# Kernel optimization log

Measured on AMD Instinct MI355X. Metric: run time of the kernel, lower is better.

Reference implementation:

```python
import jax, jax.numpy as jnp
import numpy as np

N_FACTORS = (50, 50, 50)   # vocab factorization, prod = 125000
EMB_STD = (0.5 / 512) ** (1.0 / 3.0)   # per-core std so full embedding std ~= 0.5/embedding_dim
CTX_STD = (1e-6) ** (1.0 / 3.0)


def _tt_gather(core1, core2, core3, idx):
    """idx: flat int array (N,). Cores: (n_k, r_in, m_k, r_out). Returns (N, m1*m2*m3)."""
    n1, n2, n3 = N_FACTORS
    i3 = idx % n3
    i2 = (idx // n3) % n2
    i1 = idx // (n2 * n3)
    N = idx.shape[0]
    g1 = core1[i1][:, 0]                  # (N, m1, r1)  (leading rank is 1)
    g2 = core2[i2]                        # (N, r1, m2, r2)
    res = jnp.einsum('bmr,brns->bmns', g1, g2).reshape(N, -1, g2.shape[-1])  # (N, m1*m2, r2)
    g3 = core3[i3]                        # (N, r2, m3, 1)
    res = jnp.einsum('bmr,brns->bmns', res, g3).reshape(N, -1)               # (N, m1*m2*m3)
    return res


def setup_inputs() -> dict:
    key = jax.random.key(0)
    ks = jax.random.split(key, 8)
    vocab = 125000
    word_indices = jax.random.randint(ks[0], (8192, 1), 0, vocab, dtype=jnp.int64 if jax.config.jax_enable_x64 else jnp.int32)
    context_indices = jax.random.randint(ks[1], (8192, 10), 0, vocab, dtype=jnp.int64 if jax.config.jax_enable_x64 else jnp.int32)
    w_core1 = jax.random.normal(ks[2], (50, 1, 8, 32), dtype=jnp.float32) * EMB_STD
    w_core2 = jax.random.normal(ks[3], (50, 32, 8, 32), dtype=jnp.float32) * EMB_STD
    w_core3 = jax.random.normal(ks[4], (50, 32, 8, 1), dtype=jnp.float32) * EMB_STD
    c_core1 = jax.random.normal(ks[5], (50, 1, 8, 32), dtype=jnp.float32) * CTX_STD
    c_core2 = jax.random.normal(ks[6], (50, 32, 8, 32), dtype=jnp.float32) * CTX_STD
    c_core3 = jax.random.normal(ks[7], (50, 32, 8, 1), dtype=jnp.float32) * CTX_STD
    return {
        'word_indices': word_indices,
        'context_indices': context_indices,
        'w_core1': w_core1, 'w_core2': w_core2, 'w_core3': w_core3,
        'c_core1': c_core1, 'c_core2': c_core2, 'c_core3': c_core3,
    }


def reference(word_indices, context_indices, w_core1, w_core2, w_core3, c_core1, c_core2, c_core3):
    # w = self.w_emb.forward(word_indices)[:, 0, :]
    w = _tt_gather(w_core1, w_core2, w_core3, word_indices[:, 0])          # (B, 512)
    # context_indices is 2-D: flatten, lookup, reshape back
    bs, num = context_indices.shape
    c = _tt_gather(c_core1, c_core2, c_core3, context_indices.reshape(-1)) # (B*num, 512)
    c = c.reshape(bs, num, -1)
    return (w, c)
```

## Files before the change

### kernel.cpp

```cpp
#include <hip/hip_runtime.h>


#define NFAC 50
#define TPAIR 2048
#define NPAIRS 2500
#define NKEYS 5000
#define MAXC 192
#define NWORD 8192
#define NCTX  81920
#define NLOOK (NWORD + NCTX)
#define NBB   ((NLOOK + 255) / 256)
#define NE2   409600

typedef short short8 __attribute__((ext_vector_type(8)));
typedef float f32x4v __attribute__((ext_vector_type(4)));
typedef unsigned short us4 __attribute__((ext_vector_type(4)));

__device__ __forceinline__ unsigned short f2bf(float f) {
    unsigned u = __builtin_bit_cast(unsigned, f);
    u += 0x7FFFu + ((u >> 16) & 1u);
    return (unsigned short)(u >> 16);
}

__device__ __forceinline__ int pair_of(int idx) {
    const int i3 = idx % NFAC;
    const int i2 = (idx / NFAC) % NFAC;
    return i2 * NFAC + i3;
}


__global__ __launch_bounds__(256) void tt_bucket(
    const int* __restrict__ widx, const int* __restrict__ cidx,
    const float* __restrict__ w1, const float* __restrict__ c1,
    const float* __restrict__ w2, const float* __restrict__ c2,
    const float* __restrict__ w3, const float* __restrict__ c3,
    int* __restrict__ hist, unsigned* __restrict__ bucket,
    unsigned short* __restrict__ g1w, unsigned short* __restrict__ g1c,
    unsigned short* __restrict__ g2w, unsigned short* __restrict__ g2c,
    unsigned short* __restrict__ g3w, unsigned short* __restrict__ g3c)
{
    const int b = blockIdx.x;
    const int t = threadIdx.x;
    if (b < NBB) {
        const int g = b * 256 + t;
        const int idx = (g < NWORD) ? widx[g] : cidx[g - NWORD];
        const int key = (g < NWORD ? 0 : NPAIRS) + pair_of(idx);
        const int i1  = idx / (NFAC * NFAC);
        const int pos = atomicAdd(&hist[key], 1);
        if (pos < MAXC)
            bucket[(size_t)key * MAXC + pos] = (unsigned)g | ((unsigned)i1 << 17);
        return;
    }
    if (b < NBB + 800) {
        const int gid = (b - NBB) * 256 + t;
        const int e = gid * 4;
        const float* src; unsigned short* dst; int off;
        if (e < NE2) { src = w2; dst = g2w; off = e; }
        else         { src = c2; dst = g2c; off = e - NE2; }
        const float4 v = *reinterpret_cast<const float4*>(src + off);
        us4 o; o[0] = f2bf(v.x); o[1] = f2bf(v.y); o[2] = f2bf(v.z); o[3] = f2bf(v.w);
        *reinterpret_cast<us4*>(dst + off) = o;
        return;
    }
    if (b < NBB + 900) {
        const int g = (b - NBB - 800) * 256 + t;
        if (g < 12800) g1w[g] = f2bf(w1[g]);
        else           g1c[g - 12800] = f2bf(c1[g - 12800]);
        return;
    }
    {
        const int g = (b - NBB - 900) * 256 + t;
        const int tab = g / 25600;
        const int rem = g - tab * 25600;
        const int i3 = rem >> 9, le = rem & 511;
        const int l = le >> 3, j = le & 7;
        const int col = l & 15, k = 8 * (l >> 4) + j;
        const float* src = tab ? c3 : w3;
        unsigned short* dst = tab ? g3c : g3w;
        dst[i3 * 512 + le] = (col < 8) ? f2bf(src[i3 * 256 + k * 8 + col]) : 0;
    }
}


__global__ __launch_bounds__(256, 8) void tt_group_fused(
    const unsigned* __restrict__ bucket, const int* __restrict__ hist,
    const unsigned short* __restrict__ g1w, const unsigned short* __restrict__ g1c,
    const unsigned short* __restrict__ g2w, const unsigned short* __restrict__ g2c,
    const unsigned short* __restrict__ g3w, const unsigned short* __restrict__ g3c,
    float* __restrict__ out)
{
    const int B = blockIdx.x;
    const int swz = (B & 7) * (NKEYS / 8) + (B >> 3);
    const int key = (swz & 1) ? ((swz >> 1) + NPAIRS) : (swz >> 1);

    int count = hist[key];
    if (count == 0) return;
    if (count > MAXC) count = MAXC;

    const bool isCtx = key >= NPAIRS;
    const int pair = isCtx ? key - NPAIRS : key;
    const unsigned short* g1t = isCtx ? g1c : g1w;
    const unsigned short* g2t = isCtx ? g2c : g2w;
    const unsigned short* g3t = isCtx ? g3c : g3w;
    const unsigned* kb = bucket + (size_t)key * MAXC;
    const int i2 = pair / NFAC, i3 = pair % NFAC;

    __shared__ unsigned short tl[TPAIR];
    const int t = threadIdx.x;
    const int wave = t >> 6;
    const int lane = t & 63;
    const int l15 = lane & 15;
    const int kg  = lane >> 4;

    {
        const short8 bg3 = *reinterpret_cast<const short8*>(g3t + i3 * 512 + lane * 8);
        const unsigned short* g2p = g2t + i2 * 8192;
        #pragma unroll
        for (int tile = 0; tile < 4; ++tile) {
            const int rbase = wave * 64 + tile * 16;
            const short8 a = *reinterpret_cast<const short8*>(
                g2p + (rbase + l15) * 32 + kg * 8);
            const f32x4v z = {0.f, 0.f, 0.f, 0.f};
            const f32x4v d = __builtin_amdgcn_mfma_f32_16x16x32_bf16(a, bg3, z, 0, 0, 0);
            if (l15 < 8) {
                const int p = l15;
                #pragma unroll
                for (int q = 0; q < 4; ++q) {
                    const int rn = rbase + kg * 4 + q;
                    const int r = rn >> 3, n = rn & 7;
                    const int np = n * 8 + p;
                    const int flat = (np & 3) * 512 + ((r >> 3) * 16 + (np >> 2)) * 8 + (r & 7);
                    tl[flat] = f2bf(d[q]);
                }
            }
        }
    }
    __syncthreads();

    const short8 b0 = *reinterpret_cast<const short8*>(&tl[0 * 512 + lane * 8]);
    const short8 b1 = *reinterpret_cast<const short8*>(&tl[1 * 512 + lane * 8]);
    const short8 b2 = *reinterpret_cast<const short8*>(&tl[2 * 512 + lane * 8]);
    const short8 b3 = *reinterpret_cast<const short8*>(&tl[3 * 512 + lane * 8]);

    const int sel = (lane >> 3) & 1;
    const int am  = lane & 7;

    const int ntile = (count + 1) >> 1;
    for (int jt = wave; jt < ntile; jt += 4) {
        const int j0 = 2 * jt;
        const bool has2 = (j0 + 1) < count;
        const unsigned pk0 = __builtin_amdgcn_readfirstlane(kb[j0]);
        const unsigned pk1 = has2 ? __builtin_amdgcn_readfirstlane(kb[j0 + 1]) : pk0;
        const int lid0 = pk0 & 0x1FFFF, i10 = pk0 >> 17;
        const int lid1 = pk1 & 0x1FFFF, i11 = pk1 >> 17;

        const short8 a = *reinterpret_cast<const short8*>(
            g1t + (sel ? i11 : i10) * 256 + am * 32 + kg * 8);

        const f32x4v z = {0.f, 0.f, 0.f, 0.f};
        const f32x4v d0 = __builtin_amdgcn_mfma_f32_16x16x32_bf16(a, b0, z, 0, 0, 0);
        const f32x4v d1 = __builtin_amdgcn_mfma_f32_16x16x32_bf16(a, b1, z, 0, 0, 0);
        const f32x4v d2 = __builtin_amdgcn_mfma_f32_16x16x32_bf16(a, b2, z, 0, 0, 0);
        const f32x4v d3 = __builtin_amdgcn_mfma_f32_16x16x32_bf16(a, b3, z, 0, 0, 0);

        float* o0 = out + (size_t)lid0 * 512;
        float* o1 = out + (size_t)lid1 * 512;
        #pragma unroll
        for (int q = 0; q < 4; ++q) {
            const int row = kg * 4 + q;
            const int mm = row & 7;
            float* ob = (row >= 8) ? o1 : o0;
            if (row < 8 || has2) {
                f32x4v v; v[0] = d0[q]; v[1] = d1[q]; v[2] = d2[q]; v[3] = d3[q];
                __builtin_nontemporal_store(v, (f32x4v*)(ob + mm * 64 + 4 * l15));
            }
        }
    }
}


__global__ __launch_bounds__(512) void tt_fused(
    const int* __restrict__ word_idx, const int* __restrict__ ctx_idx,
    const float* __restrict__ w1, const float* __restrict__ w2, const float* __restrict__ w3,
    const float* __restrict__ c1, const float* __restrict__ c2, const float* __restrict__ c3,
    float* __restrict__ out)
{
    const int b = blockIdx.x;
    int idx; const float *k1, *k2, *k3; float* o;
    if (b < NWORD) { idx = word_idx[b]; k1 = w1; k2 = w2; k3 = w3; o = out + (size_t)b * 512; }
    else { const int c = b - NWORD; idx = ctx_idx[c]; k1 = c1; k2 = c2; k3 = c3;
           o = out + (size_t)(NWORD + c) * 512; }
    const int i3 = idx % NFAC;
    const int rem = idx / NFAC;
    const int i2 = rem % NFAC;
    const int i1 = rem / NFAC;

    __shared__ float g3s[256];
    __shared__ float g1s[256];
    __shared__ float Ts[TPAIR];
    const int t = threadIdx.x;
    if (t < 256) g3s[t] = k3[i3 * 256 + t];
    else         g1s[t - 256] = k1[i1 * 256 + (t - 256)];
    __syncthreads();

    {
        const int e0 = t * 4;
        const int r = e0 >> 6, n = (e0 >> 3) & 7, p0 = e0 & 7;
        const float* g2row = k2 + i2 * 8192 + r * 256 + n * 32;
        float acc[4] = {0.f,0.f,0.f,0.f};
        #pragma unroll
        for (int s = 0; s < 32; ++s) {
            const float v = g2row[s];
            #pragma unroll
            for (int j = 0; j < 4; ++j) acc[j] += v * g3s[s * 8 + p0 + j];
        }
        reinterpret_cast<float4*>(Ts + e0)[0] = make_float4(acc[0], acc[1], acc[2], acc[3]);
    }
    __syncthreads();

    const int m = t >> 6, np = t & 63;
    float acc = 0.f;
    #pragma unroll
    for (int r = 0; r < 32; ++r)
        acc += g1s[m * 32 + r] * Ts[r * 64 + np];
    o[m * 64 + np] = acc;
}

extern "C" void kernel_launch(void* const* d_in, const int* in_sizes, int n_in,
                              void* d_out, int out_size, void* d_ws, size_t ws_size,
                              hipStream_t stream) {
    const int*   widx = (const int*)d_in[0];
    const int*   cidx = (const int*)d_in[1];
    const float* w1   = (const float*)d_in[2];
    const float* w2   = (const float*)d_in[3];
    const float* w3   = (const float*)d_in[4];
    const float* c1   = (const float*)d_in[5];
    const float* c2   = (const float*)d_in[6];
    const float* c3   = (const float*)d_in[7];
    float* out = (float*)d_out;

    const size_t need = 896000 * 2 + NKEYS * 4 + (size_t)NKEYS * MAXC * 4;

    if (ws_size >= need) {
        unsigned short* g1wb = (unsigned short*)d_ws;
        unsigned short* g1cb = g1wb + 12800;
        unsigned short* g2wb = g1cb + 12800;
        unsigned short* g2cb = g2wb + NE2;
        unsigned short* g3wb = g2cb + NE2;
        unsigned short* g3cb = g3wb + 25600;
        int*      hist   = (int*)(g3cb + 25600);
        unsigned* bucket = (unsigned*)(hist + NKEYS);

        hipMemsetAsync(hist, 0, NKEYS * sizeof(int), stream);
        tt_bucket<<<NBB + 1100, 256, 0, stream>>>(
            widx, cidx, w1, c1, w2, c2, w3, c3,
            hist, bucket, g1wb, g1cb, g2wb, g2cb, g3wb, g3cb);
        tt_group_fused<<<NKEYS, 256, 0, stream>>>(
            bucket, hist, g1wb, g1cb, g2wb, g2cb, g3wb, g3cb, out);
    } else {
        tt_fused<<<NLOOK, 512, 0, stream>>>(widx, cidx, w1, w2, w3, c1, c2, c3, out);
    }
}
```

Measured before the change: 61.86 us.

## Fuse memset, bucketing and grouped compute into one cooperative kernel with grid syncs

```diff
diff --git a/kernel.cpp b/kernel.cpp
--- a/kernel.cpp
+++ b/kernel.cpp
@@ -1,4 +1,5 @@
 #include <hip/hip_runtime.h>
+#include <hip/hip_cooperative_groups.h>
 
 
 #define NFAC 50
@@ -11,10 +12,14 @@
 #define NLOOK (NWORD + NCTX)
 #define NBB   ((NLOOK + 255) / 256)
 #define NE2   409600
+#define NVB   (NBB + 1100)
+#define KPX   (NKEYS / 8)
 
 typedef short short8 __attribute__((ext_vector_type(8)));
 typedef float f32x4v __attribute__((ext_vector_type(4)));
 typedef unsigned short us4 __attribute__((ext_vector_type(4)));
+
+namespace cg = cooperative_groups;
 
 __device__ __forceinline__ unsigned short f2bf(float f) {
     unsigned u = __builtin_bit_cast(unsigned, f);
@@ -29,30 +34,25 @@
 }
 
 
-__global__ __launch_bounds__(256) void tt_bucket(
-    const int* __restrict__ widx, const int* __restrict__ cidx,
-    const float* __restrict__ w1, const float* __restrict__ c1,
-    const float* __restrict__ w2, const float* __restrict__ c2,
-    const float* __restrict__ w3, const float* __restrict__ c3,
-    int* __restrict__ hist, unsigned* __restrict__ bucket,
-    unsigned short* __restrict__ g1w, unsigned short* __restrict__ g1c,
-    unsigned short* __restrict__ g2w, unsigned short* __restrict__ g2c,
-    unsigned short* __restrict__ g3w, unsigned short* __restrict__ g3c)
-{
-    const int b = blockIdx.x;
-    const int t = threadIdx.x;
-    if (b < NBB) {
-        const int g = b * 256 + t;
+__device__ __forceinline__ void do_p1(int vb, int t,
+    const int* widx, const int* cidx,
+    const float* w1, const float* c1, const float* w2, const float* c2,
+    const float* w3, const float* c3,
+    int* hist, unsigned* bucket,
+    unsigned short* g1w, unsigned short* g1c,
+    unsigned short* g2w, unsigned short* g2c,
+    unsigned short* g3w, unsigned short* g3c)
+{
+    if (vb < NBB) {
+        const int g = vb * 256 + t;
         const int idx = (g < NWORD) ? widx[g] : cidx[g - NWORD];
         const int key = (g < NWORD ? 0 : NPAIRS) + pair_of(idx);
         const int i1  = idx / (NFAC * NFAC);
         const int pos = atomicAdd(&hist[key], 1);
         if (pos < MAXC)
             bucket[(size_t)key * MAXC + pos] = (unsigned)g | ((unsigned)i1 << 17);
-        return;
-    }
-    if (b < NBB + 800) {
-        const int gid = (b - NBB) * 256 + t;
+    } else if (vb < NBB + 800) {
+        const int gid = (vb - NBB) * 256 + t;
         const int e = gid * 4;
         const float* src; unsigned short* dst; int off;
         if (e < NE2) { src = w2; dst = g2w; off = e; }
@@ -60,16 +60,12 @@
         const float4 v = *reinterpret_cast<const float4*>(src + off);
         us4 o; o[0] = f2bf(v.x); o[1] = f2bf(v.y); o[2] = f2bf(v.z); o[3] = f2bf(v.w);
         *reinterpret_cast<us4*>(dst + off) = o;
-        return;
-    }
-    if (b < NBB + 900) {
-        const int g = (b - NBB - 800) * 256 + t;
+    } else if (vb < NBB + 900) {
+        const int g = (vb - NBB - 800) * 256 + t;
         if (g < 12800) g1w[g] = f2bf(w1[g]);
         else           g1c[g - 12800] = f2bf(c1[g - 12800]);
-        return;
-    }
-    {
-        const int g = (b - NBB - 900) * 256 + t;
+    } else {
+        const int g = (vb - NBB - 900) * 256 + t;
         const int tab = g / 25600;
         const int rem = g - tab * 25600;
         const int i3 = rem >> 9, le = rem & 511;
@@ -81,21 +77,23 @@
     }
 }
 
-
-__global__ __launch_bounds__(256, 8) void tt_group_fused(
-    const unsigned* __restrict__ bucket, const int* __restrict__ hist,
-    const unsigned short* __restrict__ g1w, const unsigned short* __restrict__ g1c,
-    const unsigned short* __restrict__ g2w, const unsigned short* __restrict__ g2c,
-    const unsigned short* __restrict__ g3w, const unsigned short* __restrict__ g3c,
-    float* __restrict__ out)
-{
-    const int B = blockIdx.x;
-    const int swz = (B & 7) * (NKEYS / 8) + (B >> 3);
-    const int key = (swz & 1) ? ((swz >> 1) + NPAIRS) : (swz >> 1);
-
+__device__ __forceinline__ void do_key(int key, int t, unsigned short* tl,
+    const unsigned* bucket, const int* hist,
+    const unsigned short* g1w, const unsigned short* g1c,
+    const unsigned short* g2w, const unsigned short* g2c,
+    const unsigned short* g3w, const unsigned short* g3c,
+    float* out)
+{
     int count = hist[key];
     if (count == 0) return;
     if (count > MAXC) count = MAXC;
+
+    const int wave = t >> 6;
+    const int lane = t & 63;
+    const int l15 = lane & 15;
+    const int kg  = lane >> 4;
+    const int sel = (lane >> 3) & 1;
+    const int am  = lane & 7;
 
     const bool isCtx = key >= NPAIRS;
     const int pair = isCtx ? key - NPAIRS : key;
@@ -104,13 +102,6 @@
     const unsigned short* g3t = isCtx ? g3c : g3w;
     const unsigned* kb = bucket + (size_t)key * MAXC;
     const int i2 = pair / NFAC, i3 = pair % NFAC;
-
-    __shared__ unsigned short tl[TPAIR];
-    const int t = threadIdx.x;
-    const int wave = t >> 6;
-    const int lane = t & 63;
-    const int l15 = lane & 15;
-    const int kg  = lane >> 4;
 
     {
         const short8 bg3 = *reinterpret_cast<const short8*>(g3t + i3 * 512 + lane * 8);
@@ -141,16 +132,15 @@
     const short8 b1 = *reinterpret_cast<const short8*>(&tl[1 * 512 + lane * 8]);
     const short8 b2 = *reinterpret_cast<const short8*>(&tl[2 * 512 + lane * 8]);
     const short8 b3 = *reinterpret_cast<const short8*>(&tl[3 * 512 + lane * 8]);
-
-    const int sel = (lane >> 3) & 1;
-    const int am  = lane & 7;
+    __syncthreads();
 
     const int ntile = (count + 1) >> 1;
     for (int jt = wave; jt < ntile; jt += 4) {
         const int j0 = 2 * jt;
         const bool has2 = (j0 + 1) < count;
-        const unsigned pk0 = __builtin_amdgcn_readfirstlane(kb[j0]);
-        const unsigned pk1 = has2 ? __builtin_amdgcn_readfirstlane(kb[j0 + 1]) : pk0;
+        const uint2 pk = *reinterpret_cast<const uint2*>(kb + j0);
+        const unsigned pk0 = __builtin_amdgcn_readfirstlane(pk.x);
+        const unsigned pk1 = has2 ? __builtin_amdgcn_readfirstlane(pk.y) : pk0;
         const int lid0 = pk0 & 0x1FFFF, i10 = pk0 >> 17;
         const int lid1 = pk1 & 0x1FFFF, i11 = pk1 >> 17;
 
@@ -179,6 +169,68 @@
 }
 
 
+__global__ __launch_bounds__(256, 8) void tt_all(
+    const int* __restrict__ widx, const int* __restrict__ cidx,
+    const float* __restrict__ w1, const float* __restrict__ c1,
+    const float* __restrict__ w2, const float* __restrict__ c2,
+    const float* __restrict__ w3, const float* __restrict__ c3,
+    int* __restrict__ hist, unsigned* __restrict__ bucket,
+    unsigned short* __restrict__ g1w, unsigned short* __restrict__ g1c,
+    unsigned short* __restrict__ g2w, unsigned short* __restrict__ g2c,
+    unsigned short* __restrict__ g3w, unsigned short* __restrict__ g3c,
+    float* __restrict__ out)
+{
+    cg::grid_group grid = cg::this_grid();
+    const int b = blockIdx.x;
+    const int t = threadIdx.x;
+    const int G = gridDim.x;
+
+    for (int g = b * 256 + t; g < NKEYS; g += G * 256) hist[g] = 0;
+    grid.sync();
+
+    for (int vb = b; vb < NVB; vb += G)
+        do_p1(vb, t, widx, cidx, w1, c1, w2, c2, w3, c3,
+              hist, bucket, g1w, g1c, g2w, g2c, g3w, g3c);
+    grid.sync();
+
+    __shared__ unsigned short tl[TPAIR];
+    for (int v = b; v < NKEYS; v += G) {
+        const int swz = (v & 7) * KPX + (v >> 3);
+        const int key = (swz & 1) ? ((swz >> 1) + NPAIRS) : (swz >> 1);
+        do_key(key, t, tl, bucket, hist, g1w, g1c, g2w, g2c, g3w, g3c, out);
+    }
+}
+
+
+__global__ __launch_bounds__(256) void tt_bucket(
+    const int* __restrict__ widx, const int* __restrict__ cidx,
+    const float* __restrict__ w1, const float* __restrict__ c1,
+    const float* __restrict__ w2, const float* __restrict__ c2,
+    const float* __restrict__ w3, const float* __restrict__ c3,
+    int* __restrict__ hist, unsigned* __restrict__ bucket,
+    unsigned short* __restrict__ g1w, unsigned short* __restrict__ g1c,
+    unsigned short* __restrict__ g2w, unsigned short* __restrict__ g2c,
+    unsigned short* __restrict__ g3w, unsigned short* __restrict__ g3c)
+{
+    do_p1(blockIdx.x, threadIdx.x, widx, cidx, w1, c1, w2, c2, w3, c3,
+          hist, bucket, g1w, g1c, g2w, g2c, g3w, g3c);
+}
+
+__global__ __launch_bounds__(256, 8) void tt_group_fused(
+    const unsigned* __restrict__ bucket, const int* __restrict__ hist,
+    const unsigned short* __restrict__ g1w, const unsigned short* __restrict__ g1c,
+    const unsigned short* __restrict__ g2w, const unsigned short* __restrict__ g2c,
+    const unsigned short* __restrict__ g3w, const unsigned short* __restrict__ g3c,
+    float* __restrict__ out)
+{
+    __shared__ unsigned short tl[TPAIR];
+    const int B = blockIdx.x;
+    const int swz = (B & 7) * KPX + (B >> 3);
+    const int key = (swz & 1) ? ((swz >> 1) + NPAIRS) : (swz >> 1);
+    do_key(key, threadIdx.x, tl, bucket, hist, g1w, g1c, g2w, g2c, g3w, g3c, out);
+}
+
+
 __global__ __launch_bounds__(512) void tt_fused(
     const int* __restrict__ word_idx, const int* __restrict__ ctx_idx,
     const float* __restrict__ w1, const float* __restrict__ w2, const float* __restrict__ w3,
@@ -240,24 +292,43 @@
     float* out = (float*)d_out;
 
     const size_t need = 896000 * 2 + NKEYS * 4 + (size_t)NKEYS * MAXC * 4;
-
-    if (ws_size >= need) {
-        unsigned short* g1wb = (unsigned short*)d_ws;
-        unsigned short* g1cb = g1wb + 12800;
-        unsigned short* g2wb = g1cb + 12800;
-        unsigned short* g2cb = g2wb + NE2;
-        unsigned short* g3wb = g2cb + NE2;
-        unsigned short* g3cb = g3wb + 25600;
-        int*      hist   = (int*)(g3cb + 25600);
-        unsigned* bucket = (unsigned*)(hist + NKEYS);
-
+    if (ws_size < need) {
+        tt_fused<<<NLOOK, 512, 0, stream>>>(widx, cidx, w1, w2, w3, c1, c2, c3, out);
+        return;
+    }
+
+    unsigned short* g1wb = (unsigned short*)d_ws;
+    unsigned short* g1cb = g1wb + 12800;
+    unsigned short* g2wb = g1cb + 12800;
+    unsigned short* g2cb = g2wb + NE2;
+    unsigned short* g3wb = g2cb + NE2;
+    unsigned short* g3cb = g3wb + 25600;
+    int*      hist   = (int*)(g3cb + 25600);
+    unsigned* bucket = (unsigned*)(hist + NKEYS);
+
+    int occ = 0;
+    hipError_t qe = hipOccupancyMaxActiveBlocksPerMultiprocessor(&occ, tt_all, 256, 0);
+    bool coop_ok = false;
+    if (qe == hipSuccess && occ > 0) {
+        int grid = occ * 256;
+        if (grid > 2048) grid = 2048;
+        void* args[] = {
+            (void*)&widx, (void*)&cidx,
+            (void*)&w1, (void*)&c1, (void*)&w2, (void*)&c2, (void*)&w3, (void*)&c3,
+            (void*)&hist, (void*)&bucket,
+            (void*)&g1wb, (void*)&g1cb, (void*)&g2wb, (void*)&g2cb,
+            (void*)&g3wb, (void*)&g3cb, (void*)&out };
+        hipError_t le = hipLaunchCooperativeKernel((const void*)tt_all,
+                                                   dim3(grid), dim3(256),
+                                                   args, 0, stream);
+        coop_ok = (le == hipSuccess);
+    }
+    if (!coop_ok) {
         hipMemsetAsync(hist, 0, NKEYS * sizeof(int), stream);
-        tt_bucket<<<NBB + 1100, 256, 0, stream>>>(
-            widx, cidx, w1, c1, w2, c2, w3, c3,
-            hist, bucket, g1wb, g1cb, g2wb, g2cb, g3wb, g3cb);
-        tt_group_fused<<<NKEYS, 256, 0, stream>>>(
-            bucket, hist, g1wb, g1cb, g2wb, g2cb, g3wb, g3cb, out);
-    } else {
-        tt_fused<<<NLOOK, 512, 0, stream>>>(widx, cidx, w1, w2, w3, c1, c2, c3, out);
-    }
-}
+        tt_bucket<<<NVB, 256, 0, stream>>>(widx, cidx, w1, c1, w2, c2, w3, c3,
+                                           hist, bucket, g1wb, g1cb, g2wb, g2cb,
+                                           g3wb, g3cb);
+        tt_group_fused<<<NKEYS, 256, 0, stream>>>(bucket, hist, g1wb, g1cb,
+                                                  g2wb, g2cb, g3wb, g3cb, out);
+    }
+}
```

Measured after the change: 220.8 us. 3.57x slower.

## Process word and context buckets of a pair in one block with prefetched bucket entries

Applied to the files above, without the earlier changes.

```diff
diff --git a/kernel.cpp b/kernel.cpp
--- a/kernel.cpp
+++ b/kernel.cpp
@@ -11,6 +11,8 @@
 #define NLOOK (NWORD + NCTX)
 #define NBB   ((NLOOK + 255) / 256)
 #define NE2   409600
+#define NVB   (NBB + 1100)
+#define GG2   2504
 
 typedef short short8 __attribute__((ext_vector_type(8)));
 typedef float f32x4v __attribute__((ext_vector_type(4)));
@@ -39,20 +41,18 @@
     unsigned short* __restrict__ g2w, unsigned short* __restrict__ g2c,
     unsigned short* __restrict__ g3w, unsigned short* __restrict__ g3c)
 {
-    const int b = blockIdx.x;
+    const int vb = blockIdx.x;
     const int t = threadIdx.x;
-    if (b < NBB) {
-        const int g = b * 256 + t;
+    if (vb < NBB) {
+        const int g = vb * 256 + t;
         const int idx = (g < NWORD) ? widx[g] : cidx[g - NWORD];
         const int key = (g < NWORD ? 0 : NPAIRS) + pair_of(idx);
         const int i1  = idx / (NFAC * NFAC);
         const int pos = atomicAdd(&hist[key], 1);
         if (pos < MAXC)
             bucket[(size_t)key * MAXC + pos] = (unsigned)g | ((unsigned)i1 << 17);
-        return;
-    }
-    if (b < NBB + 800) {
-        const int gid = (b - NBB) * 256 + t;
+    } else if (vb < NBB + 800) {
+        const int gid = (vb - NBB) * 256 + t;
         const int e = gid * 4;
         const float* src; unsigned short* dst; int off;
         if (e < NE2) { src = w2; dst = g2w; off = e; }
@@ -60,16 +60,12 @@
         const float4 v = *reinterpret_cast<const float4*>(src + off);
         us4 o; o[0] = f2bf(v.x); o[1] = f2bf(v.y); o[2] = f2bf(v.z); o[3] = f2bf(v.w);
         *reinterpret_cast<us4*>(dst + off) = o;
-        return;
-    }
-    if (b < NBB + 900) {
-        const int g = (b - NBB - 800) * 256 + t;
+    } else if (vb < NBB + 900) {
+        const int g = (vb - NBB - 800) * 256 + t;
         if (g < 12800) g1w[g] = f2bf(w1[g]);
         else           g1c[g - 12800] = f2bf(c1[g - 12800]);
-        return;
-    }
-    {
-        const int g = (b - NBB - 900) * 256 + t;
+    } else {
+        const int g = (vb - NBB - 900) * 256 + t;
         const int tab = g / 25600;
         const int rem = g - tab * 25600;
         const int i3 = rem >> 9, le = rem & 511;
@@ -82,7 +78,7 @@
 }
 
 
-__global__ __launch_bounds__(256, 8) void tt_group_fused(
+__global__ __launch_bounds__(256, 8) void tt_group2(
     const unsigned* __restrict__ bucket, const int* __restrict__ hist,
     const unsigned short* __restrict__ g1w, const unsigned short* __restrict__ g1c,
     const unsigned short* __restrict__ g2w, const unsigned short* __restrict__ g2c,
@@ -90,29 +86,36 @@
     float* __restrict__ out)
 {
     const int B = blockIdx.x;
-    const int swz = (B & 7) * (NKEYS / 8) + (B >> 3);
-    const int key = (swz & 1) ? ((swz >> 1) + NPAIRS) : (swz >> 1);
-
-    int count = hist[key];
-    if (count == 0) return;
-    if (count > MAXC) count = MAXC;
-
-    const bool isCtx = key >= NPAIRS;
-    const int pair = isCtx ? key - NPAIRS : key;
-    const unsigned short* g1t = isCtx ? g1c : g1w;
-    const unsigned short* g2t = isCtx ? g2c : g2w;
-    const unsigned short* g3t = isCtx ? g3c : g3w;
-    const unsigned* kb = bucket + (size_t)key * MAXC;
-    const int i2 = pair / NFAC, i3 = pair % NFAC;
-
-    __shared__ unsigned short tl[TPAIR];
+    const int swz = (B & 7) * (GG2 / 8) + (B >> 3);
+    if (swz >= NPAIRS) return;
+    const int p = swz;
+    const int i2 = p / NFAC, i3 = p % NFAC;
+
     const int t = threadIdx.x;
     const int wave = t >> 6;
     const int lane = t & 63;
     const int l15 = lane & 15;
     const int kg  = lane >> 4;
-
-    {
+    const int sel = (lane >> 3) & 1;
+    const int am  = lane & 7;
+
+    __shared__ unsigned short tl[2][TPAIR];
+
+    int cnt[2];
+    cnt[0] = hist[p];
+    cnt[1] = hist[p + NPAIRS];
+    if (cnt[0] > MAXC) cnt[0] = MAXC;
+    if (cnt[1] > MAXC) cnt[1] = MAXC;
+    const unsigned* kbW = bucket + (size_t)p * MAXC;
+    const unsigned* kbC = bucket + (size_t)(p + NPAIRS) * MAXC;
+    uint2 pre[2] = {make_uint2(0u, 0u), make_uint2(0u, 0u)};
+    if (wave < ((cnt[0] + 1) >> 1)) pre[0] = *reinterpret_cast<const uint2*>(kbW + 2 * wave);
+    if (wave < ((cnt[1] + 1) >> 1)) pre[1] = *reinterpret_cast<const uint2*>(kbC + 2 * wave);
+
+    #pragma unroll
+    for (int tab = 0; tab < 2; ++tab) {
+        const unsigned short* g2t = tab ? g2c : g2w;
+        const unsigned short* g3t = tab ? g3c : g3w;
         const short8 bg3 = *reinterpret_cast<const short8*>(g3t + i3 * 512 + lane * 8);
         const unsigned short* g2p = g2t + i2 * 8192;
         #pragma unroll
@@ -123,57 +126,67 @@
             const f32x4v z = {0.f, 0.f, 0.f, 0.f};
             const f32x4v d = __builtin_amdgcn_mfma_f32_16x16x32_bf16(a, bg3, z, 0, 0, 0);
             if (l15 < 8) {
-                const int p = l15;
+                const int pp = l15;
                 #pragma unroll
                 for (int q = 0; q < 4; ++q) {
                     const int rn = rbase + kg * 4 + q;
                     const int r = rn >> 3, n = rn & 7;
-                    const int np = n * 8 + p;
+                    const int np = n * 8 + pp;
                     const int flat = (np & 3) * 512 + ((r >> 3) * 16 + (np >> 2)) * 8 + (r & 7);
-                    tl[flat] = f2bf(d[q]);
+                    tl[tab][flat] = f2bf(d[q]);
                 }
             }
         }
     }
     __syncthreads();
 
-    const short8 b0 = *reinterpret_cast<const short8*>(&tl[0 * 512 + lane * 8]);
-    const short8 b1 = *reinterpret_cast<const short8*>(&tl[1 * 512 + lane * 8]);
-    const short8 b2 = *reinterpret_cast<const short8*>(&tl[2 * 512 + lane * 8]);
-    const short8 b3 = *reinterpret_cast<const short8*>(&tl[3 * 512 + lane * 8]);
-
-    const int sel = (lane >> 3) & 1;
-    const int am  = lane & 7;
-
-    const int ntile = (count + 1) >> 1;
-    for (int jt = wave; jt < ntile; jt += 4) {
-        const int j0 = 2 * jt;
-        const bool has2 = (j0 + 1) < count;
-        const unsigned pk0 = __builtin_amdgcn_readfirstlane(kb[j0]);
-        const unsigned pk1 = has2 ? __builtin_amdgcn_readfirstlane(kb[j0 + 1]) : pk0;
-        const int lid0 = pk0 & 0x1FFFF, i10 = pk0 >> 17;
-        const int lid1 = pk1 & 0x1FFFF, i11 = pk1 >> 17;
-
-        const short8 a = *reinterpret_cast<const short8*>(
-            g1t + (sel ? i11 : i10) * 256 + am * 32 + kg * 8);
-
-        const f32x4v z = {0.f, 0.f, 0.f, 0.f};
-        const f32x4v d0 = __builtin_amdgcn_mfma_f32_16x16x32_bf16(a, b0, z, 0, 0, 0);
-        const f32x4v d1 = __builtin_amdgcn_mfma_f32_16x16x32_bf16(a, b1, z, 0, 0, 0);
-        const f32x4v d2 = __builtin_amdgcn_mfma_f32_16x16x32_bf16(a, b2, z, 0, 0, 0);
-        const f32x4v d3 = __builtin_amdgcn_mfma_f32_16x16x32_bf16(a, b3, z, 0, 0, 0);
-
-        float* o0 = out + (size_t)lid0 * 512;
-        float* o1 = out + (size_t)lid1 * 512;
-        #pragma unroll
-        for (int q = 0; q < 4; ++q) {
-            const int row = kg * 4 + q;
-            const int mm = row & 7;
-            float* ob = (row >= 8) ? o1 : o0;
-            if (row < 8 || has2) {
-                f32x4v v; v[0] = d0[q]; v[1] = d1[q]; v[2] = d2[q]; v[3] = d3[q];
-                __builtin_nontemporal_store(v, (f32x4v*)(ob + mm * 64 + 4 * l15));
+    #pragma unroll
+    for (int tab = 0; tab < 2; ++tab) {
+        const int count = cnt[tab];
+        if (count == 0) continue;
+        const unsigned short* g1t = tab ? g1c : g1w;
+        const unsigned* kb = tab ? kbC : kbW;
+
+        const short8 b0 = *reinterpret_cast<const short8*>(&tl[tab][0 * 512 + lane * 8]);
+        const short8 b1 = *reinterpret_cast<const short8*>(&tl[tab][1 * 512 + lane * 8]);
+        const short8 b2 = *reinterpret_cast<const short8*>(&tl[tab][2 * 512 + lane * 8]);
+        const short8 b3 = *reinterpret_cast<const short8*>(&tl[tab][3 * 512 + lane * 8]);
+
+        const int ntile = (count + 1) >> 1;
+        uint2 pkc = pre[tab];
+        for (int jt = wave; jt < ntile; jt += 4) {
+            const int jn = jt + 4;
+            uint2 pkn = pkc;
+            if (jn < ntile) pkn = *reinterpret_cast<const uint2*>(kb + 2 * jn);
+
+            const bool has2 = (2 * jt + 1) < count;
+            const unsigned pk0 = __builtin_amdgcn_readfirstlane(pkc.x);
+            const unsigned pk1 = has2 ? __builtin_amdgcn_readfirstlane(pkc.y) : pk0;
+            const int lid0 = pk0 & 0x1FFFF, i10 = pk0 >> 17;
+            const int lid1 = pk1 & 0x1FFFF, i11 = pk1 >> 17;
+
+            const short8 a = *reinterpret_cast<const short8*>(
+                g1t + (sel ? i11 : i10) * 256 + am * 32 + kg * 8);
+
+            const f32x4v z = {0.f, 0.f, 0.f, 0.f};
+            const f32x4v d0 = __builtin_amdgcn_mfma_f32_16x16x32_bf16(a, b0, z, 0, 0, 0);
+            const f32x4v d1 = __builtin_amdgcn_mfma_f32_16x16x32_bf16(a, b1, z, 0, 0, 0);
+            const f32x4v d2 = __builtin_amdgcn_mfma_f32_16x16x32_bf16(a, b2, z, 0, 0, 0);
+            const f32x4v d3 = __builtin_amdgcn_mfma_f32_16x16x32_bf16(a, b3, z, 0, 0, 0);
+
+            float* o0 = out + (size_t)lid0 * 512;
+            float* o1 = out + (size_t)lid1 * 512;
+            #pragma unroll
+            for (int q = 0; q < 4; ++q) {
+                const int row = kg * 4 + q;
+                const int mm = row & 7;
+                float* ob = (row >= 8) ? o1 : o0;
+                if (row < 8 || has2) {
+                    f32x4v v; v[0] = d0[q]; v[1] = d1[q]; v[2] = d2[q]; v[3] = d3[q];
+                    __builtin_nontemporal_store(v, (f32x4v*)(ob + mm * 64 + 4 * l15));
+                }
             }
+            pkc = pkn;
         }
     }
 }
@@ -252,11 +265,11 @@
         unsigned* bucket = (unsigned*)(hist + NKEYS);
 
         hipMemsetAsync(hist, 0, NKEYS * sizeof(int), stream);
-        tt_bucket<<<NBB + 1100, 256, 0, stream>>>(
-            widx, cidx, w1, c1, w2, c2, w3, c3,
-            hist, bucket, g1wb, g1cb, g2wb, g2cb, g3wb, g3cb);
-        tt_group_fused<<<NKEYS, 256, 0, stream>>>(
-            bucket, hist, g1wb, g1cb, g2wb, g2cb, g3wb, g3cb, out);
+        tt_bucket<<<NVB, 256, 0, stream>>>(widx, cidx, w1, c1, w2, c2, w3, c3,
+                                           hist, bucket, g1wb, g1cb, g2wb, g2cb,
+                                           g3wb, g3cb);
+        tt_group2<<<GG2, 256, 0, stream>>>(bucket, hist, g1wb, g1cb,
+                                           g2wb, g2cb, g3wb, g3cb, out);
     } else {
         tt_fused<<<NLOOK, 512, 0, stream>>>(widx, cidx, w1, w2, w3, c1, c2, c3, out);
     }
```

Result: slower. 63.51 us (+2.7%).
